# Kernel optimization log

Hardware: AMD Instinct MI355X
Metric: run time of the kernel (lower is better)

## Reference

```python
import jax, jax.numpy as jnp
import numpy as np

B, T, D, H, NB = 16, 256, 1024, 16, 6
V, GD, MLP_H, FF_H = 401000, 300, 2048, 4096
NEG = float(-(2**32) + 1)  # Kyubyong-style large negative padding (finite, avoids NaNs)


def _ln(x, g, b, eps=1e-8):
    m = x.mean(-1, keepdims=True)
    v = x.var(-1, keepdims=True)
    return (x - m) / jnp.sqrt(v + eps) * g + b


def setup_inputs() -> dict:
    key = jax.random.key(0)
    ks = jax.random.split(key, 16)
    rn = lambda i, shape: jax.random.normal(ks[i], shape, jnp.float32) * 0.02
    graph = jax.random.randint(ks[2], (B, T, T), 0, 2).astype(jnp.int32)
    graph = jnp.maximum(graph, jnp.eye(T, dtype=jnp.int32)[None])  # self-edges so no fully-masked query row
    return {
        'syb_ipt': jax.random.randint(ks[0], (B, T), 0, V),
        'syb_mask': jax.random.randint(ks[1], (B, T), 0, 2).astype(jnp.int32),
        'syb_graph': graph,
        'emb_table': rn(3, (V, GD)),
        'mlp_w1': rn(4, (GD, MLP_H)), 'mlp_b1': jnp.zeros((MLP_H,), jnp.float32),
        'mlp_w2': rn(5, (MLP_H, D)), 'mlp_b2': jnp.zeros((D,), jnp.float32),
        'pos_table': rn(6, (T, D)),
        'wq': rn(7, (NB, D, D)), 'bq': jnp.zeros((NB, D), jnp.float32),
        'wk': rn(8, (NB, D, D)), 'bk': jnp.zeros((NB, D), jnp.float32),
        'wv': rn(9, (NB, D, D)), 'bv': jnp.zeros((NB, D), jnp.float32),
        'ln1_g': jnp.ones((NB, D), jnp.float32), 'ln1_b': jnp.zeros((NB, D), jnp.float32),
        'ff_w1': rn(10, (NB, D, FF_H)), 'ff_b1': jnp.zeros((NB, FF_H), jnp.float32),
        'ff_w2': rn(11, (NB, FF_H, D)), 'ff_b2': jnp.zeros((NB, D), jnp.float32),
        'ln2_g': jnp.ones((NB, D), jnp.float32), 'ln2_b': jnp.zeros((NB, D), jnp.float32),
    }


def reference(syb_ipt, syb_mask, syb_graph, emb_table, mlp_w1, mlp_b1, mlp_w2, mlp_b2,
              pos_table, wq, bq, wk, bk, wv, bv, ln1_g, ln1_b,
              ff_w1, ff_b1, ff_w2, ff_b2, ln2_g, ln2_b):
    b, t = syb_ipt.shape
    dh = D // H
    scale = float(np.sqrt(dh))
    # embedding lookup + 2-layer MLP + positional add (dropout = identity in eval)
    x = emb_table[syb_ipt]                                        # (B,T,300)
    x = jax.nn.relu(x @ mlp_w1 + mlp_b1) @ mlp_w2 + mlp_b2        # (B,T,D)
    x = x + pos_table[None, :t]
    kmask = syb_mask > 0                                          # (B,T)
    gmask = syb_graph > 0                                         # (B,T,T)
    qscale = syb_mask.astype(x.dtype)[:, None, :, None]           # query masking
    for i in range(NB):
        q = jax.nn.relu(x @ wq[i] + bq[i]).reshape(b, t, H, dh)
        k = jax.nn.relu(x @ wk[i] + bk[i]).reshape(b, t, H, dh)
        v = jax.nn.relu(x @ wv[i] + bv[i]).reshape(b, t, H, dh)
        s = jnp.einsum('bqhd,bkhd->bhqk', q, k) / scale           # (B,H,T,T)
        s = jnp.where(kmask[:, None, None, :], s, NEG)            # key (padding) mask
        s = jnp.where(gmask[:, None], s, NEG)                     # graph mask bias
        a = jax.nn.softmax(s, axis=-1) * qscale
        o = jnp.einsum('bhqk,bkhd->bqhd', a, v).reshape(b, t, D)
        x = _ln(o + x, ln1_g[i], ln1_b[i])                        # residual + layernorm
        h = jax.nn.relu(x @ ff_w1[i] + ff_b1[i]) @ ff_w2[i] + ff_b2[i]
        x = _ln(h + x, ln2_g[i], ln2_b[i])
    return x
```

## Files before the change

### kernel.cpp

```cpp
#include <hip/hip_runtime.h>
#include <hip/hip_bf16.h>
#include <math.h>

#define B_    16
#define T_    256
#define D_    1024
#define H_    16
#define DH_   64
#define NB_   6
#define GD_   300
#define GDP_  320
#define MLPH_ 2048
#define FFH_  4096
#define NTOK  (B_ * T_)
#define NEGV  -4294967296.0f

typedef __hip_bfloat16 bf16;
typedef __attribute__((ext_vector_type(8))) short short8;
typedef __attribute__((ext_vector_type(4))) float floatx4;

__device__ __forceinline__ unsigned short f2b(float v) {
    __hip_bfloat16 h = __float2bfloat16(v);
    return __builtin_bit_cast(unsigned short, h);
}
__device__ __forceinline__ float b2f(unsigned short u) {
    union { unsigned i; float f; } x; x.i = ((unsigned)u) << 16; return x.f;
}

__device__ __forceinline__ void gld16(const void* g, void* l) {
    __builtin_amdgcn_global_load_lds(
        (const __attribute__((address_space(1))) unsigned int*)g,
        (__attribute__((address_space(3))) unsigned int*)(uintptr_t)l,
        16, 0, 0);
}

__global__ __launch_bounds__(256)
void convT_kernel(const float* __restrict__ W, bf16* __restrict__ WT,
                  int K, int N, int Kpad, size_t strideIn, size_t strideOut)
{
    __shared__ float t[32][33];
    const float* Wb = W + (size_t)blockIdx.z * strideIn;
    bf16* WTb = WT + (size_t)blockIdx.z * strideOut;
    int n0 = blockIdx.x * 32, k0 = blockIdx.y * 32;
    int tx = threadIdx.x & 31, ty = threadIdx.x >> 5;
#pragma unroll
    for (int r = 0; r < 4; r++) {
        int k = k0 + ty + r * 8;
        t[ty + r * 8][tx] = (k < K) ? Wb[(size_t)k * N + n0 + tx] : 0.f;
    }
    __syncthreads();
#pragma unroll
    for (int r = 0; r < 4; r++) {
        int n = n0 + ty + r * 8;
        WTb[(size_t)n * Kpad + k0 + tx] = __float2bfloat16(t[tx][ty + r * 8]);
    }
}

__global__ __launch_bounds__(256)
void gather_kernel(const int* __restrict__ ipt, const float* __restrict__ emb,
                   bf16* __restrict__ out)
{
    int row = blockIdx.x;
    int v = ipt[row];
    const float* src = emb + (size_t)v * GD_;
    bf16* dst = out + (size_t)row * GDP_;
    for (int c = threadIdx.x; c < GDP_; c += blockDim.x)
        dst[c] = (c < GD_) ? __float2bfloat16(src[c]) : __float2bfloat16(0.f);
}

__global__ __launch_bounds__(256)
void gbias_kernel(const int* __restrict__ mask, const int* __restrict__ graph,
                  bf16* __restrict__ gb)
{
    int r = blockIdx.x;
    int b = r >> 8;
    int k = threadIdx.x;
    int ok = mask[b * T_ + k] & graph[(size_t)r * T_ + k];
    gb[(size_t)r * T_ + k] = __float2bfloat16(ok ? 0.f : NEGV);
}

__global__ __launch_bounds__(256)
void bcat_kernel(const float* __restrict__ bq, const float* __restrict__ bk,
                 const float* __restrict__ bv, float* __restrict__ out)
{
    int i = blockIdx.x;
    int j = blockIdx.y * 256 + threadIdx.x;
    float v = (j < 1024) ? bq[i * 1024 + j]
            : (j < 2048) ? bk[i * 1024 + j - 1024]
                         : bv[i * 1024 + j - 2048];
    out[i * 3072 + j] = v;
}

template<bool RELU, bool ADDPOS, bool DUAL, bool QKVQ, typename OutT>
__global__ __launch_bounds__(256)
void mm_bf16(const bf16* __restrict__ A, const bf16* __restrict__ BT,
             const float* __restrict__ bias, const float* __restrict__ pos,
             OutT* __restrict__ C, bf16* __restrict__ C2,
             int M, int N, int K)
{
    __shared__ __align__(16) short lsA[8192];
    __shared__ __align__(16) short lsB[8192];
    const int tid = threadIdx.x;
    const int wv = tid >> 6, ln = tid & 63;
    const int m0 = blockIdx.y * 128, n0 = blockIdx.x * 128;
    const int wm = (wv >> 1) * 64, wn = (wv & 1) * 64;
    const int ml = ln & 15, q = ln >> 4;

    floatx4 acc[4][4] = {};

    const int cbase[4] = { (0 * 4 + wv) * 64, (1 * 4 + wv) * 64, (2 * 4 + wv) * 64, (3 * 4 + wv) * 64 };
    int srow[4], skc[4];
#pragma unroll
    for (int p = 0; p < 4; p++) {
        int c = cbase[p] + ln;
        srow[p] = c >> 3;
        skc[p] = (c & 7) ^ (srow[p] & 7);
    }

    for (int kt = 0; kt < K; kt += 64) {
#pragma unroll
        for (int p = 0; p < 4; p++) {
            const bf16* ga = A + (size_t)(m0 + srow[p]) * K + kt + skc[p] * 8;
            const bf16* gb = BT + (size_t)(n0 + srow[p]) * K + kt + skc[p] * 8;
            gld16(ga, &lsA[cbase[p] * 8]);
            gld16(gb, &lsB[cbase[p] * 8]);
        }
        __syncthreads();

        short8 af[4][2], bfr[4][2];
#pragma unroll
        for (int i = 0; i < 4; i++) {
#pragma unroll
            for (int ks = 0; ks < 2; ks++) {
                int r = wm + i * 16 + ml;
                int kc = ks * 4 + q;
                af[i][ks] = *(const short8*)&lsA[(r * 8 + (kc ^ (r & 7))) * 8];
                int n = wn + i * 16 + ml;
                bfr[i][ks] = *(const short8*)&lsB[(n * 8 + (kc ^ (n & 7))) * 8];
            }
        }
#pragma unroll
        for (int ks = 0; ks < 2; ks++)
#pragma unroll
            for (int i = 0; i < 4; i++)
#pragma unroll
                for (int j = 0; j < 4; j++)
                    acc[i][j] = __builtin_amdgcn_mfma_f32_16x16x32_bf16(
                        af[i][ks], bfr[j][ks], acc[i][j], 0, 0, 0);
        __syncthreads();
    }

#pragma unroll
    for (int i = 0; i < 4; i++) {
#pragma unroll
        for (int j = 0; j < 4; j++) {
            int col = n0 + wn + j * 16 + ml;
            float bb = bias[col];
            float sc = (QKVQ && col < D_) ? 0.125f : 1.0f;
#pragma unroll
            for (int rg = 0; rg < 4; rg++) {
                int row = m0 + wm + i * 16 + q * 4 + rg;
                float v = acc[i][j][rg] + bb;
                if (ADDPOS) v += pos[(size_t)(row & (T_ - 1)) * N + col];
                if (RELU) v = fmaxf(v, 0.f);
                if (QKVQ) v *= sc;
                size_t idx = (size_t)row * N + col;
                if constexpr (sizeof(OutT) == 4) C[idx] = v;
                else C[idx] = (OutT)__float2bfloat16(v);
                if (DUAL) C2[idx] = __float2bfloat16(v);
            }
        }
    }
}

__global__ __launch_bounds__(256, 2)
void attn2_kernel(const bf16* __restrict__ QKV, const bf16* __restrict__ gbias,
                  const int* __restrict__ mask, float* __restrict__ O)
{
    __shared__ unsigned short lds[32768];
    const int tid = threadIdx.x;
    const int wv = tid >> 6, ln = tid & 63;
    const int ml = ln & 15, qq = ln >> 4;
    const int qc = blockIdx.x & 3;
    const int h  = (blockIdx.x >> 2) & 15;
    const int b  = blockIdx.x >> 6;
    const int tok0 = b * T_;

    const unsigned short* QKVu = (const unsigned short*)QKV;

#pragma unroll
    for (int it = 0; it < 4; it++) {
        int k = (tid >> 2) + it * 64;
        int d0 = (tid & 3) * 16;
        const unsigned short* src = QKVu + (size_t)(tok0 + k) * 3072 + 2048 + h * 64 + d0;
        union { uint4 u[2]; unsigned short s[16]; } v;
        v.u[0] = *(const uint4*)src;
        v.u[1] = *(const uint4*)(src + 8);
#pragma unroll
        for (int e = 0; e < 16; e++) {
            int d = d0 + e;
            lds[d * 256 + (((k >> 3) ^ (d & 7)) << 3) + (k & 7)] = v.s[e];
        }
    }

    const int q0 = qc * 64 + wv * 16;
    short8 qa[2];
#pragma unroll
    for (int ks = 0; ks < 2; ks++)
        qa[ks] = *(const short8*)(QKVu + (size_t)(tok0 + q0 + ml) * 3072 + h * 64 + ks * 32 + qq * 8);

    __syncthreads();

    floatx4 sb[16] = {};
#pragma unroll
    for (int jt = 0; jt < 16; jt++) {
        const unsigned short* kr = QKVu + (size_t)(tok0 + jt * 16 + ml) * 3072 + 1024 + h * 64 + qq * 8;
        short8 kb0 = *(const short8*)kr;
        short8 kb1 = *(const short8*)(kr + 32);
        sb[jt] = __builtin_amdgcn_mfma_f32_16x16x32_bf16(qa[0], kb0, sb[jt], 0, 0, 0);
        sb[jt] = __builtin_amdgcn_mfma_f32_16x16x32_bf16(qa[1], kb1, sb[jt], 0, 0, 0);
    }

    const unsigned short* gb = (const unsigned short*)gbias + (size_t)(tok0 + q0) * T_;
#pragma unroll
    for (int jt = 0; jt < 16; jt++)
#pragma unroll
        for (int r = 0; r < 4; r++)
            sb[jt][r] += b2f(gb[(size_t)(qq * 4 + r) * T_ + jt * 16 + ml]);

    float mx[4];
#pragma unroll
    for (int r = 0; r < 4; r++) {
        float m = sb[0][r];
#pragma unroll
        for (int jt = 1; jt < 16; jt++) m = fmaxf(m, sb[jt][r]);
#pragma unroll
        for (int off = 1; off < 16; off <<= 1) m = fmaxf(m, __shfl_xor(m, off, 64));
        mx[r] = m;
    }
    float lsum[4] = {0.f, 0.f, 0.f, 0.f};
    unsigned short* Pw = lds + 16384 + wv * 4096;
#pragma unroll
    for (int jt = 0; jt < 16; jt++) {
#pragma unroll
        for (int r = 0; r < 4; r++) {
            float e = __expf(sb[jt][r] - mx[r]);
            lsum[r] += e;
            int row = qq * 4 + r;
            int k = jt * 16 + ml;
            Pw[row * 256 + (((k >> 3) ^ (row & 7)) << 3) + (k & 7)] = f2b(e);
        }
    }
#pragma unroll
    for (int r = 0; r < 4; r++)
#pragma unroll
        for (int off = 1; off < 16; off <<= 1) lsum[r] += __shfl_xor(lsum[r], off, 64);

    __syncthreads();

    floatx4 oa[4] = {};
    const unsigned short* Pr = lds + 16384 + wv * 4096;
#pragma unroll
    for (int ks = 0; ks < 8; ks++) {
        short8 pa = *(const short8*)&Pr[ml * 256 + (((ks * 4 + qq) ^ (ml & 7)) << 3)];
#pragma unroll
        for (int jd = 0; jd < 4; jd++) {
            int n = jd * 16 + ml;
            short8 vb = *(const short8*)&lds[n * 256 + (((ks * 4 + qq) ^ (n & 7)) << 3)];
            oa[jd] = __builtin_amdgcn_mfma_f32_16x16x32_bf16(pa, vb, oa[jd], 0, 0, 0);
        }
    }

    float fin[4];
#pragma unroll
    for (int r = 0; r < 4; r++) {
        int row = q0 + qq * 4 + r;
        fin[r] = (float)mask[tok0 + row] / lsum[r];
    }
#pragma unroll
    for (int jd = 0; jd < 4; jd++)
#pragma unroll
        for (int r = 0; r < 4; r++) {
            int row = q0 + qq * 4 + r;
            O[(size_t)(tok0 + row) * D_ + h * 64 + jd * 16 + ml] = oa[jd][r] * fin[r];
        }
}

__global__ __launch_bounds__(256)
void add_ln_kernel(const float* __restrict__ Xin, const float* __restrict__ Yin,
                   const float* __restrict__ g, const float* __restrict__ beta,
                   float* __restrict__ Out, bf16* __restrict__ Outb)
{
    const int row = blockIdx.x;
    const int tid = threadIdx.x;
    const float4 a = ((const float4*)(Xin + (size_t)row * D_))[tid];
    const float4 b = ((const float4*)(Yin + (size_t)row * D_))[tid];
    float v0 = a.x + b.x, v1 = a.y + b.y, v2 = a.z + b.z, v3 = a.w + b.w;

    __shared__ float red[8];
    float lsum = v0 + v1 + v2 + v3;
#pragma unroll
    for (int off = 32; off > 0; off >>= 1) lsum += __shfl_xor(lsum, off, 64);
    int wave = tid >> 6;
    if ((tid & 63) == 0) red[wave] = lsum;
    __syncthreads();
    float mean = (red[0] + red[1] + red[2] + red[3]) * (1.f / (float)D_);

    float d0 = v0 - mean, d1 = v1 - mean, d2 = v2 - mean, d3 = v3 - mean;
    float ls2 = d0 * d0 + d1 * d1 + d2 * d2 + d3 * d3;
#pragma unroll
    for (int off = 32; off > 0; off >>= 1) ls2 += __shfl_xor(ls2, off, 64);
    if ((tid & 63) == 0) red[4 + wave] = ls2;
    __syncthreads();
    float var = (red[4] + red[5] + red[6] + red[7]) * (1.f / (float)D_);
    float inv = 1.f / sqrtf(var + 1e-8f);

    int col = tid * 4;
    float4 gv = *(const float4*)(g + col);
    float4 bv = *(const float4*)(beta + col);
    float4 o;
    o.x = d0 * inv * gv.x + bv.x;
    o.y = d1 * inv * gv.y + bv.y;
    o.z = d2 * inv * gv.z + bv.z;
    o.w = d3 * inv * gv.w + bv.w;
    ((float4*)(Out + (size_t)row * D_))[tid] = o;

    union { unsigned short u[4]; uint2 v; } pk;
    pk.u[0] = f2b(o.x); pk.u[1] = f2b(o.y); pk.u[2] = f2b(o.z); pk.u[3] = f2b(o.w);
    *(uint2*)&Outb[(size_t)row * D_ + col] = pk.v;
}

extern "C" void kernel_launch(void* const* d_in, const int* in_sizes, int n_in,
                              void* d_out, int out_size, void* d_ws, size_t ws_size,
                              hipStream_t stream)
{
    const int*   syb_ipt   = (const int*)d_in[0];
    const int*   syb_mask  = (const int*)d_in[1];
    const int*   syb_graph = (const int*)d_in[2];
    const float* emb       = (const float*)d_in[3];
    const float* mlp_w1    = (const float*)d_in[4];
    const float* mlp_b1    = (const float*)d_in[5];
    const float* mlp_w2    = (const float*)d_in[6];
    const float* mlp_b2    = (const float*)d_in[7];
    const float* pos       = (const float*)d_in[8];
    const float* wq        = (const float*)d_in[9];
    const float* bq        = (const float*)d_in[10];
    const float* wk        = (const float*)d_in[11];
    const float* bk        = (const float*)d_in[12];
    const float* wv        = (const float*)d_in[13];
    const float* bv        = (const float*)d_in[14];
    const float* ln1g      = (const float*)d_in[15];
    const float* ln1b      = (const float*)d_in[16];
    const float* ffw1      = (const float*)d_in[17];
    const float* ffb1      = (const float*)d_in[18];
    const float* ffw2      = (const float*)d_in[19];
    const float* ffb2      = (const float*)d_in[20];
    const float* ln2g      = (const float*)d_in[21];
    const float* ln2b      = (const float*)d_in[22];

    char* p = (char*)d_ws;
    auto alloc = [&](size_t bytes) { char* r = p; p += (bytes + 255) & ~(size_t)255; return r; };
    float* X    = (float*)alloc((size_t)NTOK * D_ * 4);
    float* Rb   = (float*)alloc((size_t)NTOK * D_ * 4);
    bf16*  Xb   = (bf16*)alloc((size_t)NTOK * D_ * 2);
    bf16*  EMBb = (bf16*)alloc((size_t)NTOK * GDP_ * 2);
    bf16*  Hb   = (bf16*)alloc((size_t)NTOK * FFH_ * 2);
    bf16*  QKVb = (bf16*)alloc((size_t)NTOK * 3072 * 2);
    bf16*  qkvT = (bf16*)alloc((size_t)NB_ * 3072 * D_ * 2);
    bf16*  f1T  = (bf16*)alloc((size_t)NB_ * D_ * FFH_ * 2);
    bf16*  f2T  = (bf16*)alloc((size_t)NB_ * D_ * FFH_ * 2);
    bf16*  m1T  = (bf16*)alloc((size_t)MLPH_ * GDP_ * 2);
    bf16*  m2T  = (bf16*)alloc((size_t)D_ * MLPH_ * 2);
    float* bqkv = (float*)alloc((size_t)NB_ * 3072 * 4);
    bf16*  gB   = (bf16*)alloc((size_t)NTOK * T_ * 2);

    convT_kernel<<<dim3(D_ / 32, D_ / 32, NB_), 256, 0, stream>>>(
        wq, qkvT + 0, D_, D_, D_, (size_t)D_ * D_, (size_t)3072 * D_);
    convT_kernel<<<dim3(D_ / 32, D_ / 32, NB_), 256, 0, stream>>>(
        wk, qkvT + (size_t)1024 * D_, D_, D_, D_, (size_t)D_ * D_, (size_t)3072 * D_);
    convT_kernel<<<dim3(D_ / 32, D_ / 32, NB_), 256, 0, stream>>>(
        wv, qkvT + (size_t)2048 * D_, D_, D_, D_, (size_t)D_ * D_, (size_t)3072 * D_);
    convT_kernel<<<dim3(FFH_ / 32, D_ / 32, NB_), 256, 0, stream>>>(
        ffw1, f1T, D_, FFH_, D_, (size_t)D_ * FFH_, (size_t)D_ * FFH_);
    convT_kernel<<<dim3(D_ / 32, FFH_ / 32, NB_), 256, 0, stream>>>(
        ffw2, f2T, FFH_, D_, FFH_, (size_t)D_ * FFH_, (size_t)D_ * FFH_);
    convT_kernel<<<dim3(MLPH_ / 32, GDP_ / 32, 1), 256, 0, stream>>>(
        mlp_w1, m1T, GD_, MLPH_, GDP_, 0, 0);
    convT_kernel<<<dim3(D_ / 32, MLPH_ / 32, 1), 256, 0, stream>>>(
        mlp_w2, m2T, MLPH_, D_, MLPH_, 0, 0);
    bcat_kernel<<<dim3(NB_, 12), 256, 0, stream>>>(bq, bk, bv, bqkv);
    gbias_kernel<<<NTOK, 256, 0, stream>>>(syb_mask, syb_graph, gB);
    gather_kernel<<<NTOK, 256, 0, stream>>>(syb_ipt, emb, EMBb);

    mm_bf16<true, false, false, false, bf16><<<dim3(MLPH_ / 128, NTOK / 128), 256, 0, stream>>>(
        EMBb, m1T, mlp_b1, nullptr, Hb, nullptr, NTOK, MLPH_, GDP_);
    mm_bf16<false, true, true, false, float><<<dim3(D_ / 128, NTOK / 128), 256, 0, stream>>>(
        Hb, m2T, mlp_b2, pos, X, Xb, NTOK, D_, MLPH_);

    for (int i = 0; i < NB_; i++) {
        mm_bf16<true, false, false, true, bf16><<<dim3(3072 / 128, NTOK / 128), 256, 0, stream>>>(
            Xb, qkvT + (size_t)i * 3072 * D_, bqkv + (size_t)i * 3072, nullptr,
            QKVb, nullptr, NTOK, 3072, D_);

        attn2_kernel<<<B_ * H_ * 4, 256, 0, stream>>>(QKVb, gB, syb_mask, Rb);

        add_ln_kernel<<<NTOK, 256, 0, stream>>>(
            X, Rb, ln1g + (size_t)i * D_, ln1b + (size_t)i * D_, X, Xb);

        mm_bf16<true, false, false, false, bf16><<<dim3(FFH_ / 128, NTOK / 128), 256, 0, stream>>>(
            Xb, f1T + (size_t)i * D_ * FFH_, ffb1 + (size_t)i * FFH_, nullptr, Hb, nullptr, NTOK, FFH_, D_);
        mm_bf16<false, false, false, false, float><<<dim3(D_ / 128, NTOK / 128), 256, 0, stream>>>(
            Hb, f2T + (size_t)i * D_ * FFH_, ffb2 + (size_t)i * D_, nullptr, Rb, nullptr, NTOK, D_, FFH_);

        float* out_ptr = (i == NB_ - 1) ? (float*)d_out : X;
        add_ln_kernel<<<NTOK, 256, 0, stream>>>(
            X, Rb, ln2g + (size_t)i * D_, ln2b + (size_t)i * D_, out_ptr, Xb);
    }
}
```

Before: 2.230 ms.

## Split-K the N=1024 GEMMs and fuse partial reduction into layernorm

The FF2 and MLP second-layer GEMMs now split K four ways across blockIdx.z, writing fp32 partials to a new workspace buffer. The bias add and the partial reduction move into the following add+layernorm kernel, or into a new MLP finalize kernel that also adds the position embedding. This raises block count from one block per CU to four, to improve occupancy and latency hiding for long-K GEMMs. The trade-off is extra global memory traffic to write and re-read four fp32 partial tensors.

```diff
diff --git a/kernel.cpp b/kernel.cpp
--- a/kernel.cpp
+++ b/kernel.cpp
@@ -91,12 +91,12 @@
     out[i * 3072 + j] = v;
 }
 
-template<bool RELU, bool ADDPOS, bool DUAL, bool QKVQ, typename OutT>
+template<bool RELU, bool ADDPOS, bool DUAL, bool QKVQ, bool PARTIAL, typename OutT>
 __global__ __launch_bounds__(256)
 void mm_bf16(const bf16* __restrict__ A, const bf16* __restrict__ BT,
              const float* __restrict__ bias, const float* __restrict__ pos,
              OutT* __restrict__ C, bf16* __restrict__ C2,
-             int M, int N, int K)
+             int M, int N, int K, int lda)
 {
     __shared__ __align__(16) short lsA[8192];
     __shared__ __align__(16) short lsB[8192];
@@ -105,6 +105,7 @@
     const int m0 = blockIdx.y * 128, n0 = blockIdx.x * 128;
     const int wm = (wv >> 1) * 64, wn = (wv & 1) * 64;
     const int ml = ln & 15, q = ln >> 4;
+    const int koff = PARTIAL ? blockIdx.z * K : 0;
 
     floatx4 acc[4][4] = {};
 
@@ -117,11 +118,11 @@
         skc[p] = (c & 7) ^ (srow[p] & 7);
     }
 
-    for (int kt = 0; kt < K; kt += 64) {
+    for (int kt = koff; kt < koff + K; kt += 64) {
 #pragma unroll
         for (int p = 0; p < 4; p++) {
-            const bf16* ga = A + (size_t)(m0 + srow[p]) * K + kt + skc[p] * 8;
-            const bf16* gb = BT + (size_t)(n0 + srow[p]) * K + kt + skc[p] * 8;
+            const bf16* ga = A + (size_t)(m0 + srow[p]) * lda + kt + skc[p] * 8;
+            const bf16* gb = BT + (size_t)(n0 + srow[p]) * lda + kt + skc[p] * 8;
             gld16(ga, &lsA[cbase[p] * 8]);
             gld16(gb, &lsB[cbase[p] * 8]);
         }
@@ -155,19 +156,24 @@
 #pragma unroll
         for (int j = 0; j < 4; j++) {
             int col = n0 + wn + j * 16 + ml;
-            float bb = bias[col];
+            float bb = PARTIAL ? 0.f : bias[col];
             float sc = (QKVQ && col < D_) ? 0.125f : 1.0f;
 #pragma unroll
             for (int rg = 0; rg < 4; rg++) {
                 int row = m0 + wm + i * 16 + q * 4 + rg;
-                float v = acc[i][j][rg] + bb;
-                if (ADDPOS) v += pos[(size_t)(row & (T_ - 1)) * N + col];
-                if (RELU) v = fmaxf(v, 0.f);
-                if (QKVQ) v *= sc;
+                float v = acc[i][j][rg];
                 size_t idx = (size_t)row * N + col;
-                if constexpr (sizeof(OutT) == 4) C[idx] = v;
-                else C[idx] = (OutT)__float2bfloat16(v);
-                if (DUAL) C2[idx] = __float2bfloat16(v);
+                if constexpr (PARTIAL) {
+                    C[(size_t)blockIdx.z * M * N + idx] = v;
+                } else {
+                    v += bb;
+                    if (ADDPOS) v += pos[(size_t)(row & (T_ - 1)) * N + col];
+                    if (RELU) v = fmaxf(v, 0.f);
+                    if (QKVQ) v *= sc;
+                    if constexpr (sizeof(OutT) == 4) C[idx] = v;
+                    else C[idx] = (OutT)__float2bfloat16(v);
+                    if (DUAL) C2[idx] = __float2bfloat16(v);
+                }
             }
         }
     }
@@ -328,6 +334,80 @@
     union { unsigned short u[4]; uint2 v; } pk;
     pk.u[0] = f2b(o.x); pk.u[1] = f2b(o.y); pk.u[2] = f2b(o.z); pk.u[3] = f2b(o.w);
     *(uint2*)&Outb[(size_t)row * D_ + col] = pk.v;
+}
+
+template<int NP>
+__global__ __launch_bounds__(256)
+void add_ln_red_kernel(const float* __restrict__ Xin, const float* __restrict__ P,
+                       const float* __restrict__ bias,
+                       const float* __restrict__ g, const float* __restrict__ beta,
+                       float* __restrict__ Out, bf16* __restrict__ Outb)
+{
+    const int row = blockIdx.x;
+    const int tid = threadIdx.x;
+    const int col = tid * 4;
+    const float4 a = ((const float4*)(Xin + (size_t)row * D_))[tid];
+    const float4 bs = *(const float4*)(bias + col);
+    float v0 = a.x + bs.x, v1 = a.y + bs.y, v2 = a.z + bs.z, v3 = a.w + bs.w;
+#pragma unroll
+    for (int s = 0; s < NP; s++) {
+        const float4 pp = ((const float4*)(P + (size_t)s * NTOK * D_ + (size_t)row * D_))[tid];
+        v0 += pp.x; v1 += pp.y; v2 += pp.z; v3 += pp.w;
+    }
+
+    __shared__ float red[8];
+    float lsum = v0 + v1 + v2 + v3;
+#pragma unroll
+    for (int off = 32; off > 0; off >>= 1) lsum += __shfl_xor(lsum, off, 64);
+    int wave = tid >> 6;
+    if ((tid & 63) == 0) red[wave] = lsum;
+    __syncthreads();
+    float mean = (red[0] + red[1] + red[2] + red[3]) * (1.f / (float)D_);
+
+    float d0 = v0 - mean, d1 = v1 - mean, d2 = v2 - mean, d3 = v3 - mean;
+    float ls2 = d0 * d0 + d1 * d1 + d2 * d2 + d3 * d3;
+#pragma unroll
+    for (int off = 32; off > 0; off >>= 1) ls2 += __shfl_xor(ls2, off, 64);
+    if ((tid & 63) == 0) red[4 + wave] = ls2;
+    __syncthreads();
+    float var = (red[4] + red[5] + red[6] + red[7]) * (1.f / (float)D_);
+    float inv = 1.f / sqrtf(var + 1e-8f);
+
+    float4 gv = *(const float4*)(g + col);
+    float4 bv = *(const float4*)(beta + col);
+    float4 o;
+    o.x = d0 * inv * gv.x + bv.x;
+    o.y = d1 * inv * gv.y + bv.y;
+    o.z = d2 * inv * gv.z + bv.z;
+    o.w = d3 * inv * gv.w + bv.w;
+    ((float4*)(Out + (size_t)row * D_))[tid] = o;
+
+    union { unsigned short u[4]; uint2 v; } pk;
+    pk.u[0] = f2b(o.x); pk.u[1] = f2b(o.y); pk.u[2] = f2b(o.z); pk.u[3] = f2b(o.w);
+    *(uint2*)&Outb[(size_t)row * D_ + col] = pk.v;
+}
+
+template<int NP>
+__global__ __launch_bounds__(256)
+void mlp_fin_kernel(const float* __restrict__ P, const float* __restrict__ bias,
+                    const float* __restrict__ pos, float* __restrict__ X,
+                    bf16* __restrict__ Xb)
+{
+    const int row = blockIdx.x;
+    const int tid = threadIdx.x;
+    const int col = tid * 4;
+    float4 v = *(const float4*)(bias + col);
+    const float4 pv = *(const float4*)(pos + (size_t)(row & (T_ - 1)) * D_ + col);
+    v.x += pv.x; v.y += pv.y; v.z += pv.z; v.w += pv.w;
+#pragma unroll
+    for (int s = 0; s < NP; s++) {
+        const float4 p = ((const float4*)(P + (size_t)s * NTOK * D_ + (size_t)row * D_))[tid];
+        v.x += p.x; v.y += p.y; v.z += p.z; v.w += p.w;
+    }
+    ((float4*)(X + (size_t)row * D_))[tid] = v;
+    union { unsigned short u[4]; uint2 q; } pk;
+    pk.u[0] = f2b(v.x); pk.u[1] = f2b(v.y); pk.u[2] = f2b(v.z); pk.u[3] = f2b(v.w);
+    *(uint2*)&Xb[(size_t)row * D_ + col] = pk.q;
 }
 
 extern "C" void kernel_launch(void* const* d_in, const int* in_sizes, int n_in,
@@ -373,6 +453,7 @@
     bf16*  m2T  = (bf16*)alloc((size_t)D_ * MLPH_ * 2);
     float* bqkv = (float*)alloc((size_t)NB_ * 3072 * 4);
     bf16*  gB   = (bf16*)alloc((size_t)NTOK * T_ * 2);
+    float* Pk   = (float*)alloc((size_t)4 * NTOK * D_ * 4);
 
     convT_kernel<<<dim3(D_ / 32, D_ / 32, NB_), 256, 0, stream>>>(
         wq, qkvT + 0, D_, D_, D_, (size_t)D_ * D_, (size_t)3072 * D_);
@@ -392,28 +473,30 @@
     gbias_kernel<<<NTOK, 256, 0, stream>>>(syb_mask, syb_graph, gB);
     gather_kernel<<<NTOK, 256, 0, stream>>>(syb_ipt, emb, EMBb);
 
-    mm_bf16<true, false, false, false, bf16><<<dim3(MLPH_ / 128, NTOK / 128), 256, 0, stream>>>(
-        EMBb, m1T, mlp_b1, nullptr, Hb, nullptr, NTOK, MLPH_, GDP_);
-    mm_bf16<false, true, true, false, float><<<dim3(D_ / 128, NTOK / 128), 256, 0, stream>>>(
-        Hb, m2T, mlp_b2, pos, X, Xb, NTOK, D_, MLPH_);
+    mm_bf16<true, false, false, false, false, bf16><<<dim3(MLPH_ / 128, NTOK / 128), 256, 0, stream>>>(
+        EMBb, m1T, mlp_b1, nullptr, Hb, nullptr, NTOK, MLPH_, GDP_, GDP_);
+    mm_bf16<false, false, false, false, true, float><<<dim3(D_ / 128, NTOK / 128, 4), 256, 0, stream>>>(
+        Hb, m2T, nullptr, nullptr, Pk, nullptr, NTOK, D_, MLPH_ / 4, MLPH_);
+    mlp_fin_kernel<4><<<NTOK, 256, 0, stream>>>(Pk, mlp_b2, pos, X, Xb);
 
     for (int i = 0; i < NB_; i++) {
-        mm_bf16<true, false, false, true, bf16><<<dim3(3072 / 128, NTOK / 128), 256, 0, stream>>>(
+        mm_bf16<true, false, false, true, false, bf16><<<dim3(3072 / 128, NTOK / 128), 256, 0, stream>>>(
             Xb, qkvT + (size_t)i * 3072 * D_, bqkv + (size_t)i * 3072, nullptr,
-            QKVb, nullptr, NTOK, 3072, D_);
+            QKVb, nullptr, NTOK, 3072, D_, D_);
 
         attn2_kernel<<<B_ * H_ * 4, 256, 0, stream>>>(QKVb, gB, syb_mask, Rb);
 
         add_ln_kernel<<<NTOK, 256, 0, stream>>>(
             X, Rb, ln1g + (size_t)i * D_, ln1b + (size_t)i * D_, X, Xb);
 
-        mm_bf16<true, false, false, false, bf16><<<dim3(FFH_ / 128, NTOK / 128), 256, 0, stream>>>(
-            Xb, f1T + (size_t)i * D_ * FFH_, ffb1 + (size_t)i * FFH_, nullptr, Hb, nullptr, NTOK, FFH_, D_);
-        mm_bf16<false, false, false, false, float><<<dim3(D_ / 128, NTOK / 128), 256, 0, stream>>>(
-            Hb, f2T + (size_t)i * D_ * FFH_, ffb2 + (size_t)i * D_, nullptr, Rb, nullptr, NTOK, D_, FFH_);
+        mm_bf16<true, false, false, false, false, bf16><<<dim3(FFH_ / 128, NTOK / 128), 256, 0, stream>>>(
+            Xb, f1T + (size_t)i * D_ * FFH_, ffb1 + (size_t)i * FFH_, nullptr, Hb, nullptr, NTOK, FFH_, D_, D_);
+
+        mm_bf16<false, false, false, false, true, float><<<dim3(D_ / 128, NTOK / 128, 4), 256, 0, stream>>>(
+            Hb, f2T + (size_t)i * D_ * FFH_, nullptr, nullptr, Pk, nullptr, NTOK, D_, FFH_ / 4, FFH_);
 
         float* out_ptr = (i == NB_ - 1) ? (float*)d_out : X;
-        add_ln_kernel<<<NTOK, 256, 0, stream>>>(
-            X, Rb, ln2g + (size_t)i * D_, ln2b + (size_t)i * D_, out_ptr, Xb);
-    }
-}
+        add_ln_red_kernel<4><<<NTOK, 256, 0, stream>>>(
+            X, Pk, ffb2 + (size_t)i * D_, ln2g + (size_t)i * D_, ln2b + (size_t)i * D_, out_ptr, Xb);
+    }
+}
```

Measured after the change: 2.100 ms. 1.06x faster.
